# Performance work log

Measured on AMD Instinct MI355X. Metric: run time of the kernel, lower is better.

## Reference

```python
import jax, jax.numpy as jnp
import numpy as np

N_NODES = 100000
N_EDGES = 3200000
N_FEAT = 128
N_GRAPHS = 512


def setup_inputs() -> dict:
    key = jax.random.key(0)
    ks = jax.random.split(key, 12)
    x = jax.random.normal(ks[0], (N_NODES, N_FEAT), dtype=jnp.float32)
    edge_index = jax.random.randint(ks[1], (2, N_EDGES), 0, N_NODES, dtype=jnp.int64)
    batch = jnp.sort(jax.random.randint(ks[2], (N_NODES,), 0, N_GRAPHS, dtype=jnp.int64))
    s = 0.1
    return {
        "x": x,
        "edge_index": edge_index,
        "batch": batch,
        "W1": jax.random.normal(ks[3], (N_FEAT, 64), dtype=jnp.float32) * s,
        "b1": jnp.zeros((64,), dtype=jnp.float32),
        "W2": jax.random.normal(ks[4], (64, 64), dtype=jnp.float32) * s,
        "b2": jnp.zeros((64,), dtype=jnp.float32),
        "Wl1": jax.random.normal(ks[5], (64, 32), dtype=jnp.float32) * s,
        "bl1": jnp.zeros((32,), dtype=jnp.float32),
        "Wl2": jax.random.normal(ks[6], (32, 2), dtype=jnp.float32) * s,
        "bl2": jnp.zeros((2,), dtype=jnp.float32),
    }


def gcn_conv(x, src, dst, W, b, n_nodes):
    # PyG GCNConv: linear transform first, then symmetric-normalized
    # aggregation over A + I (self loops), bias added after aggregation.
    h = x @ W  # [N, out]
    loop = jnp.arange(n_nodes, dtype=src.dtype)
    s = jnp.concatenate([src, loop])
    d = jnp.concatenate([dst, loop])
    deg = jax.ops.segment_sum(jnp.ones(d.shape, dtype=h.dtype), d, num_segments=n_nodes)
    dinv = jax.lax.rsqrt(jnp.where(deg > 0, deg, 1.0))
    norm = dinv[s] * dinv[d]  # [E+N]
    msg = h[s] * norm[:, None]  # gather + scale
    out = jax.ops.segment_sum(msg, d, num_segments=n_nodes)  # scatter-add
    return out + b


def reference(x, edge_index, batch, W1, b1, W2, b2, Wl1, bl1, Wl2, bl2):
    src, dst = edge_index[0], edge_index[1]
    h = jax.nn.relu(gcn_conv(x, src, dst, W1, b1, N_NODES))
    # dropout is identity in eval mode
    h = gcn_conv(h, src, dst, W2, b2, N_NODES)
    # global mean pool over graphs
    counts = jax.ops.segment_sum(jnp.ones((N_NODES,), dtype=h.dtype), batch, num_segments=N_GRAPHS)
    pooled = jax.ops.segment_sum(h, batch, num_segments=N_GRAPHS)
    pooled = pooled / jnp.maximum(counts, 1.0)[:, None]  # [G, 64]
    z = pooled @ Wl1 + bl1
    z = z @ Wl2 + bl2  # [G, 2]
    return jax.nn.softmax(z, axis=0)  # faithful to Softmax(dim=0)
```

## Files before the change

kernel.cpp:

```cpp
#include <hip/hip_runtime.h>
#include <hip/hip_fp16.h>
#include <math.h>

#define N_NODES 100000
#define N_EDGES 3200000
#define N_GRAPHS 512

#define BSHIFT 8
#define BSPAN 256
#define NB 391
#define SLACK 9216
#define SBLK 4096
#define SBLOCKS ((N_EDGES + SBLK - 1) / SBLK)

typedef float floatx2 __attribute__((ext_vector_type(2)));

__global__ __launch_bounds__(512) void init_kernel(int* __restrict__ cursor) {
    int tid = threadIdx.x;
    if (tid < NB) cursor[tid] = tid * SLACK;
}

__global__ __launch_bounds__(256) void scatter3_kernel(const int* __restrict__ src,
                                                       const int* __restrict__ dst,
                                                       int* __restrict__ cursor,
                                                       unsigned int* __restrict__ pairs, int E) {
    __shared__ int hcnt[NB];
    __shared__ int hbase[NB];
    int tid = threadIdx.x;
    for (int b = tid; b < NB; b += 256) hcnt[b] = 0;
    __syncthreads();
    int base = blockIdx.x * SBLK;
    int end = min(E, base + SBLK);
    int e = base + tid * 4;
    for (; e + 3 < end; e += 1024) {
        int4 d4 = *reinterpret_cast<const int4*>(&dst[e]);
        atomicAdd(&hcnt[d4.x >> BSHIFT], 1);
        atomicAdd(&hcnt[d4.y >> BSHIFT], 1);
        atomicAdd(&hcnt[d4.z >> BSHIFT], 1);
        atomicAdd(&hcnt[d4.w >> BSHIFT], 1);
    }
    for (; e < end; ++e) atomicAdd(&hcnt[dst[e] >> BSHIFT], 1);
    __syncthreads();
    for (int b = tid; b < NB; b += 256) {
        int c = hcnt[b];
        if (c) hbase[b] = atomicAdd(&cursor[b], c);
        hcnt[b] = 0;
    }
    __syncthreads();
    e = base + tid * 4;
    for (; e + 3 < end; e += 1024) {
        int4 d4 = *reinterpret_cast<const int4*>(&dst[e]);
        int4 s4 = *reinterpret_cast<const int4*>(&src[e]);
        int b0 = d4.x >> BSHIFT, b1 = d4.y >> BSHIFT, b2 = d4.z >> BSHIFT, b3 = d4.w >> BSHIFT;
        int r0 = atomicAdd(&hcnt[b0], 1);
        int r1 = atomicAdd(&hcnt[b1], 1);
        int r2 = atomicAdd(&hcnt[b2], 1);
        int r3 = atomicAdd(&hcnt[b3], 1);
        pairs[hbase[b0] + r0] = ((unsigned int)s4.x << BSHIFT) | (unsigned int)(d4.x & (BSPAN - 1));
        pairs[hbase[b1] + r1] = ((unsigned int)s4.y << BSHIFT) | (unsigned int)(d4.y & (BSPAN - 1));
        pairs[hbase[b2] + r2] = ((unsigned int)s4.z << BSHIFT) | (unsigned int)(d4.z & (BSPAN - 1));
        pairs[hbase[b3] + r3] = ((unsigned int)s4.w << BSHIFT) | (unsigned int)(d4.w & (BSPAN - 1));
    }
    for (; e < end; ++e) {
        int d = dst[e];
        int b = d >> BSHIFT;
        int rk = atomicAdd(&hcnt[b], 1);
        pairs[hbase[b] + rk] = ((unsigned int)src[e] << BSHIFT) | (unsigned int)(d & (BSPAN - 1));
    }
}

__global__ __launch_bounds__(256) void bucket_kernel(const unsigned int* __restrict__ pairs,
                                                     const int* __restrict__ cursor,
                                                     int* __restrict__ col,
                                                     int2* __restrict__ bele,
                                                     float* __restrict__ dinv, int N) {
    __shared__ int ncnt[BSPAN];
    __shared__ int nb4[BSPAN];
    __shared__ int a[BSPAN];
    int b = blockIdx.x, tid = threadIdx.x;
    int base = b * SLACK;
    int cntb = cursor[b] - base;
    int n0 = b << BSHIFT;
    int nn = min(BSPAN, N - n0);
    ncnt[tid] = 0;
    __syncthreads();
    for (int i = tid; i < cntb; i += 256)
        atomicAdd(&ncnt[pairs[base + i] & (BSPAN - 1)], 1);
    __syncthreads();
    int v = ncnt[tid];
    int pad = (v + 3) & ~3;
    a[tid] = pad;
    __syncthreads();
    for (int st = 1; st < 256; st <<= 1) {
        int t = (tid >= st) ? a[tid - st] : 0;
        __syncthreads();
        a[tid] += t;
        __syncthreads();
    }
    int excl = a[tid] - pad;
    nb4[tid] = excl;
    if (tid < nn) {
        int beg = base + excl;
        bele[n0 + tid] = make_int2(beg, beg + v);
        dinv[n0 + tid] = rsqrtf((float)(v + 1));
    }
    ncnt[tid] = 0;
    __syncthreads();
    for (int i = tid; i < cntb; i += 256) {
        unsigned int p = pairs[base + i];
        int dl = p & (BSPAN - 1);
        int pos = base + nb4[dl] + atomicAdd(&ncnt[dl], 1);
        col[pos] = (int)(p >> BSHIFT) << 3;
    }
}

__global__ __launch_bounds__(128) void wz_kernel(const float* __restrict__ W2,
                                                 const float* __restrict__ b2,
                                                 const float* __restrict__ Wl1,
                                                 const float* __restrict__ bl1,
                                                 const float* __restrict__ Wl2,
                                                 const float* __restrict__ bl2,
                                                 float* __restrict__ Wz,
                                                 float* __restrict__ zc) {
    __shared__ float Weff[64 * 2];
    int tid = threadIdx.x;
    {
        int c = tid >> 1, j = tid & 1;
        float s = 0.f;
        for (int k = 0; k < 32; ++k) s += Wl1[c * 32 + k] * Wl2[k * 2 + j];
        Weff[c * 2 + j] = s;
    }
    __syncthreads();
    {
        int i = tid >> 1, j = tid & 1;
        float s = 0.f;
        for (int c = 0; c < 64; ++c) s += W2[i * 64 + c] * Weff[c * 2 + j];
        Wz[i * 2 + j] = s;
    }
    if (tid < 2) {
        float s = bl2[tid];
        for (int k = 0; k < 32; ++k) s += bl1[k] * Wl2[k * 2 + tid];
        for (int c = 0; c < 64; ++c) s += b2[c] * Weff[c * 2 + tid];
        zc[tid] = s;
    }
}

template <int K>
__global__ __launch_bounds__(256) void lin_kernel(const float* __restrict__ X,
                                                  const float* __restrict__ W,
                                                  const float* __restrict__ rs,
                                                  unsigned char* __restrict__ U) {
    __shared__ float Ws[K * 64];
    __shared__ float Xs[32 * K];
    int tid = threadIdx.x;
    for (int i = tid * 4; i < K * 64; i += 256 * 4)
        *reinterpret_cast<float4*>(&Ws[i]) = *reinterpret_cast<const float4*>(&W[i]);
    int row0 = blockIdx.x * 32;
    const float* Xbase = X + (size_t)row0 * K;
    for (int i = tid * 4; i < 32 * K; i += 256 * 4)
        *reinterpret_cast<float4*>(&Xs[i]) = *reinterpret_cast<const float4*>(&Xbase[i]);
    __syncthreads();

    int wid = tid >> 6, lane = tid & 63;
    int rbase = wid * 8;
    float acc[8];
#pragma unroll
    for (int r = 0; r < 8; ++r) acc[r] = 0.f;

    for (int k4 = 0; k4 < K / 4; ++k4) {
        float w0 = Ws[(k4 * 4 + 0) * 64 + lane];
        float w1 = Ws[(k4 * 4 + 1) * 64 + lane];
        float w2 = Ws[(k4 * 4 + 2) * 64 + lane];
        float w3 = Ws[(k4 * 4 + 3) * 64 + lane];
#pragma unroll
        for (int r = 0; r < 8; ++r) {
            float4 xv = *reinterpret_cast<const float4*>(&Xs[(rbase + r) * K + k4 * 4]);
            acc[r] += xv.x * w0 + xv.y * w1 + xv.z * w2 + xv.w * w3;
        }
    }
#pragma unroll
    for (int r = 0; r < 8; ++r) {
        int row = row0 + rbase + r;
        float v = acc[r] * rs[row];
        int pk = __builtin_amdgcn_cvt_pk_fp8_f32(v, v, 0, false);
        U[(size_t)row * 64 + lane] = (unsigned char)(pk & 0xff);
    }
}

#define ACC8(a)                                                                  \
    {                                                                            \
        acc2[0] += __builtin_amdgcn_cvt_pk_f32_fp8((int)(a).x, false);           \
        acc2[1] += __builtin_amdgcn_cvt_pk_f32_fp8((int)(a).x, true);            \
        acc2[2] += __builtin_amdgcn_cvt_pk_f32_fp8((int)(a).y, false);           \
        acc2[3] += __builtin_amdgcn_cvt_pk_f32_fp8((int)(a).y, true);            \
    }

__global__ __launch_bounds__(256) void agg1_kernel(const unsigned char* __restrict__ u,
                                                   const int2* __restrict__ bele,
                                                   const int* __restrict__ col,
                                                   const float* __restrict__ dinv,
                                                   const float* __restrict__ bias,
                                                   const float* __restrict__ Wz,
                                                   float2* __restrict__ qz, int n) {
    __shared__ float Wz0s[64];
    __shared__ float Wz1s[64];
    int tid = threadIdx.x;
    if (tid < 64) Wz0s[tid] = Wz[tid * 2];
    else if (tid < 128) Wz1s[tid - 64] = Wz[(tid - 64) * 2 + 1];
    __syncthreads();

    int wid = tid >> 6, lane = tid & 63;
    int node = blockIdx.x * 4 + wid;
    if (node >= n) return;
    int r = lane >> 3, c = lane & 7;
    unsigned int c8 = (unsigned int)c * 8;

    int2 be = bele[node];
    int beg = be.x, end = be.y;
    floatx2 acc2[4];
#pragma unroll
    for (int j = 0; j < 4; ++j) acc2[j] = (floatx2)(0.f);

    int e = beg + r * 4;
    while (e + 3 < end) {
        int4 c4 = *reinterpret_cast<const int4*>(&col[e]);
        uint2 a0 = *reinterpret_cast<const uint2*>(u + (((unsigned int)c4.x << 3) + c8));
        uint2 a1 = *reinterpret_cast<const uint2*>(u + (((unsigned int)c4.y << 3) + c8));
        uint2 a2 = *reinterpret_cast<const uint2*>(u + (((unsigned int)c4.z << 3) + c8));
        uint2 a3 = *reinterpret_cast<const uint2*>(u + (((unsigned int)c4.w << 3) + c8));
        ACC8(a0); ACC8(a1); ACC8(a2); ACC8(a3);
        e += 32;
    }
#pragma unroll
    for (int k = 0; k < 4; ++k) {
        int ee = e + k;
        if (ee < end) {
            uint2 a0 = *reinterpret_cast<const uint2*>(u + (((unsigned int)col[ee] << 3) + c8));
            ACC8(a0);
        }
    }
#pragma unroll
    for (int m = 8; m <= 32; m <<= 1) {
#pragma unroll
        for (int j = 0; j < 4; ++j) {
            acc2[j].x += __shfl_xor(acc2[j].x, m);
            acc2[j].y += __shfl_xor(acc2[j].y, m);
        }
    }
    if (r == 0) {
        unsigned int vs = ((unsigned int)node << 6) + c8;
        uint2 sfr = *reinterpret_cast<const uint2*>(u + vs);
        ACC8(sfr);
        float di = dinv[node];
        float4 b0 = *reinterpret_cast<const float4*>(&bias[c * 8]);
        float4 b1 = *reinterpret_cast<const float4*>(&bias[c * 8 + 4]);
        float o[8];
#pragma unroll
        for (int j = 0; j < 4; ++j) {
            o[2 * j]     = di * acc2[j].x;
            o[2 * j + 1] = di * acc2[j].y;
        }
        o[0] += b0.x; o[1] += b0.y; o[2] += b0.z; o[3] += b0.w;
        o[4] += b1.x; o[5] += b1.y; o[6] += b1.z; o[7] += b1.w;
#pragma unroll
        for (int j = 0; j < 8; ++j) o[j] = fmaxf(o[j], 0.f);
        float p0 = 0.f, p1 = 0.f;
#pragma unroll
        for (int j = 0; j < 8; ++j) {
            p0 += o[j] * Wz0s[c * 8 + j];
            p1 += o[j] * Wz1s[c * 8 + j];
        }
#pragma unroll
        for (int m = 1; m <= 4; m <<= 1) {
            p0 += __shfl_xor(p0, m);
            p1 += __shfl_xor(p1, m);
        }
        if (lane == 0) qz[node] = make_float2(p0 * di, p1 * di);
    }
}

__global__ __launch_bounds__(256) void agg2q_kernel(const float2* __restrict__ qz,
                                                    const int2* __restrict__ bele,
                                                    const int* __restrict__ col,
                                                    const float* __restrict__ dinv,
                                                    float* __restrict__ pooled2,
                                                    const int* __restrict__ batch, int n) {
    __shared__ float2 sh[16];
    __shared__ int sg[16];
    int tid = threadIdx.x;
    int wid = tid >> 6, lane = tid & 63;
    int sub = lane >> 4, slot = lane & 15;
    int li = wid * 4 + sub;
    int node = blockIdx.x * 16 + li;
    bool valid = node < n;

    float ax = 0.f, ay = 0.f;
    if (valid) {
        int2 be = bele[node];
        const char* qb = (const char*)qz;
        int e = be.x + slot;
        while (e + 16 < be.y) {
            float2 v0 = *reinterpret_cast<const float2*>(qb + (unsigned int)col[e]);
            float2 v1 = *reinterpret_cast<const float2*>(qb + (unsigned int)col[e + 16]);
            ax += v0.x + v1.x; ay += v0.y + v1.y;
            e += 32;
        }
        if (e < be.y) {
            float2 v0 = *reinterpret_cast<const float2*>(qb + (unsigned int)col[e]);
            ax += v0.x; ay += v0.y;
        }
    }
#pragma unroll
    for (int m = 1; m <= 8; m <<= 1) {
        ax += __shfl_xor(ax, m);
        ay += __shfl_xor(ay, m);
    }
    if (slot == 0) {
        if (valid) {
            float2 self = qz[node];
            float di = dinv[node];
            sh[li] = make_float2(di * (ax + self.x), di * (ay + self.y));
            sg[li] = batch[node];
        } else {
            sh[li] = make_float2(0.f, 0.f);
            sg[li] = -1;
        }
    }
    __syncthreads();
    if (tid < 2) {
        float s = 0.f;
        int gp = -1;
        for (int w = 0; w < 16; ++w) {
            int g = sg[w];
            if (g < 0) continue;
            if (g != gp) {
                if (gp >= 0) atomicAdd(&pooled2[gp * 2 + tid], s);
                s = 0.f;
                gp = g;
            }
            s += (tid == 0) ? sh[w].x : sh[w].y;
        }
        if (gp >= 0) atomicAdd(&pooled2[gp * 2 + tid], s);
    }
}

__global__ __launch_bounds__(512) void head_kernel(const float* __restrict__ pooled2,
                                                   const int* __restrict__ batch,
                                                   const float* __restrict__ zc,
                                                   float* __restrict__ out, int N) {
    __shared__ float red[512];
    int tid = threadIdx.x;
    int g = tid;
    auto lb = [&](int key) {
        int l = 0, r = N;
        while (l < r) { int m = (l + r) >> 1; if (batch[m] < key) l = m + 1; else r = m; }
        return l;
    };
    int cnt = lb(g + 1) - lb(g);
    float cn = fmaxf((float)cnt, 1.f);
    float z0 = pooled2[g * 2 + 0] / cn + zc[0];
    float z1 = pooled2[g * 2 + 1] / cn + zc[1];

    red[tid] = z0; __syncthreads();
    for (int s = 256; s > 0; s >>= 1) { if (tid < s) red[tid] = fmaxf(red[tid], red[tid + s]); __syncthreads(); }
    float m0 = red[0]; __syncthreads();
    float e0 = expf(z0 - m0);
    red[tid] = e0; __syncthreads();
    for (int s = 256; s > 0; s >>= 1) { if (tid < s) red[tid] += red[tid + s]; __syncthreads(); }
    float s0 = red[0]; __syncthreads();
    out[g * 2 + 0] = e0 / s0;

    red[tid] = z1; __syncthreads();
    for (int s = 256; s > 0; s >>= 1) { if (tid < s) red[tid] = fmaxf(red[tid], red[tid + s]); __syncthreads(); }
    float m1 = red[0]; __syncthreads();
    float e1 = expf(z1 - m1);
    red[tid] = e1; __syncthreads();
    for (int s = 256; s > 0; s >>= 1) { if (tid < s) red[tid] += red[tid + s]; __syncthreads(); }
    float s1 = red[0]; __syncthreads();
    out[g * 2 + 1] = e1 / s1;
}

extern "C" void kernel_launch(void* const* d_in, const int* in_sizes, int n_in,
                              void* d_out, int out_size, void* d_ws, size_t ws_size,
                              hipStream_t stream) {
    const float* x   = (const float*)d_in[0];
    const int*   ei  = (const int*)d_in[1];
    const int*   bat = (const int*)d_in[2];
    const float* W1  = (const float*)d_in[3];
    const float* b1  = (const float*)d_in[4];
    const float* W2  = (const float*)d_in[5];
    const float* b2  = (const float*)d_in[6];
    const float* Wl1 = (const float*)d_in[7];
    const float* bl1 = (const float*)d_in[8];
    const float* Wl2 = (const float*)d_in[9];
    const float* bl2 = (const float*)d_in[10];
    float* out = (float*)d_out;

    const int N = N_NODES, E = N_EDGES;
    const int* src = ei;
    const int* dst = ei + E;

    size_t o = 0;
    auto alloc = [&](size_t bytes) {
        void* p = (char*)d_ws + o;
        o += (bytes + 255) / 256 * 256;
        return p;
    };
    int*           cursor  = (int*)alloc((size_t)NB * 4);
    unsigned int*  pairs   = (unsigned int*)alloc((size_t)NB * SLACK * 4 + 4096);
    int*           col     = (int*)alloc((size_t)NB * SLACK * 4 + 4096);
    int2*          bele    = (int2*)alloc((size_t)N * 8);
    float*         dinv    = (float*)alloc((size_t)N * 4);
    unsigned char* T       = (unsigned char*)alloc((size_t)N * 64);
    float2*        qz      = (float2*)alloc((size_t)N * 8);
    float*         Wz      = (float*)alloc(128 * 4);
    float*         zc      = (float*)alloc(2 * 4);
    float*         pooled2 = (float*)alloc((size_t)N_GRAPHS * 2 * 4);

    hipMemsetAsync(pooled2, 0, (size_t)N_GRAPHS * 2 * 4, stream);

    init_kernel<<<1, 512, 0, stream>>>(cursor);
    scatter3_kernel<<<SBLOCKS, 256, 0, stream>>>(src, dst, cursor, pairs, E);
    bucket_kernel<<<NB, 256, 0, stream>>>(pairs, cursor, col, bele, dinv, N);

    wz_kernel<<<1, 128, 0, stream>>>(W2, b2, Wl1, bl1, Wl2, bl2, Wz, zc);

    lin_kernel<128><<<N / 32, 256, 0, stream>>>(x, W1, dinv, T);
    agg1_kernel<<<(N + 3) / 4, 256, 0, stream>>>(T, bele, col, dinv, b1, Wz, qz, N);

    agg2q_kernel<<<(N + 15) / 16, 256, 0, stream>>>(qz, bele, col, dinv, pooled2, bat, N);

    head_kernel<<<1, 512, 0, stream>>>(pooled2, bat, zc, out, N);
}
```

Measured before the change: 225.8 us.

## Shrink CSR buckets, single-pass register-held scatter, and strided edge loop in aggregation

Halves the destination bucket span to 128 nodes (782 buckets, smaller slack), so the bucket kernel gets more blocks and less per-block work. The scatter kernel now loads dst and src once into registers and keeps the local atomic ranks, which removes the second read pass and the second round of shared atomics. Per-node column padding to multiples of 4 is dropped, and agg1 now reads edges strided by 8 across lanes instead of int4 chunks. The risks are more register pressure in scatter, a slack overflow if a bucket exceeds 4800 edges, and scalar col loads in place of vector ones.

Result: faster. 218.9 us (-3.1%).

```diff
diff --git a/kernel.cpp b/kernel.cpp
--- a/kernel.cpp
+++ b/kernel.cpp
@@ -6,18 +6,18 @@
 #define N_EDGES 3200000
 #define N_GRAPHS 512
 
-#define BSHIFT 8
-#define BSPAN 256
-#define NB 391
-#define SLACK 9216
+#define BSHIFT 7
+#define BSPAN 128
+#define NB 782
+#define SLACK 4800
 #define SBLK 4096
 #define SBLOCKS ((N_EDGES + SBLK - 1) / SBLK)
 
 typedef float floatx2 __attribute__((ext_vector_type(2)));
 
 __global__ __launch_bounds__(512) void init_kernel(int* __restrict__ cursor) {
-    int tid = threadIdx.x;
-    if (tid < NB) cursor[tid] = tid * SLACK;
+    int i = blockIdx.x * 512 + threadIdx.x;
+    if (i < NB) cursor[i] = i * SLACK;
 }
 
 __global__ __launch_bounds__(256) void scatter3_kernel(const int* __restrict__ src,
@@ -31,41 +31,45 @@
     __syncthreads();
     int base = blockIdx.x * SBLK;
     int end = min(E, base + SBLK);
-    int e = base + tid * 4;
-    for (; e + 3 < end; e += 1024) {
-        int4 d4 = *reinterpret_cast<const int4*>(&dst[e]);
-        atomicAdd(&hcnt[d4.x >> BSHIFT], 1);
-        atomicAdd(&hcnt[d4.y >> BSHIFT], 1);
-        atomicAdd(&hcnt[d4.z >> BSHIFT], 1);
-        atomicAdd(&hcnt[d4.w >> BSHIFT], 1);
-    }
-    for (; e < end; ++e) atomicAdd(&hcnt[dst[e] >> BSHIFT], 1);
+    int4 dv[4], sv[4];
+    int rk[16];
+    bool ok[4];
+#pragma unroll
+    for (int k = 0; k < 4; ++k) {
+        int e = base + tid * 4 + k * 1024;
+        ok[k] = (e < end);
+        if (ok[k]) {
+            dv[k] = *reinterpret_cast<const int4*>(&dst[e]);
+            sv[k] = *reinterpret_cast<const int4*>(&src[e]);
+        }
+    }
+#pragma unroll
+    for (int k = 0; k < 4; ++k) {
+        if (ok[k]) {
+            rk[4 * k + 0] = atomicAdd(&hcnt[dv[k].x >> BSHIFT], 1);
+            rk[4 * k + 1] = atomicAdd(&hcnt[dv[k].y >> BSHIFT], 1);
+            rk[4 * k + 2] = atomicAdd(&hcnt[dv[k].z >> BSHIFT], 1);
+            rk[4 * k + 3] = atomicAdd(&hcnt[dv[k].w >> BSHIFT], 1);
+        }
+    }
     __syncthreads();
     for (int b = tid; b < NB; b += 256) {
         int c = hcnt[b];
         if (c) hbase[b] = atomicAdd(&cursor[b], c);
-        hcnt[b] = 0;
-    }
-    __syncthreads();
-    e = base + tid * 4;
-    for (; e + 3 < end; e += 1024) {
-        int4 d4 = *reinterpret_cast<const int4*>(&dst[e]);
-        int4 s4 = *reinterpret_cast<const int4*>(&src[e]);
-        int b0 = d4.x >> BSHIFT, b1 = d4.y >> BSHIFT, b2 = d4.z >> BSHIFT, b3 = d4.w >> BSHIFT;
-        int r0 = atomicAdd(&hcnt[b0], 1);
-        int r1 = atomicAdd(&hcnt[b1], 1);
-        int r2 = atomicAdd(&hcnt[b2], 1);
-        int r3 = atomicAdd(&hcnt[b3], 1);
-        pairs[hbase[b0] + r0] = ((unsigned int)s4.x << BSHIFT) | (unsigned int)(d4.x & (BSPAN - 1));
-        pairs[hbase[b1] + r1] = ((unsigned int)s4.y << BSHIFT) | (unsigned int)(d4.y & (BSPAN - 1));
-        pairs[hbase[b2] + r2] = ((unsigned int)s4.z << BSHIFT) | (unsigned int)(d4.z & (BSPAN - 1));
-        pairs[hbase[b3] + r3] = ((unsigned int)s4.w << BSHIFT) | (unsigned int)(d4.w & (BSPAN - 1));
-    }
-    for (; e < end; ++e) {
-        int d = dst[e];
-        int b = d >> BSHIFT;
-        int rk = atomicAdd(&hcnt[b], 1);
-        pairs[hbase[b] + rk] = ((unsigned int)src[e] << BSHIFT) | (unsigned int)(d & (BSPAN - 1));
+    }
+    __syncthreads();
+#pragma unroll
+    for (int k = 0; k < 4; ++k) {
+        if (ok[k]) {
+            pairs[hbase[dv[k].x >> BSHIFT] + rk[4 * k + 0]] =
+                ((unsigned int)sv[k].x << BSHIFT) | (unsigned int)(dv[k].x & (BSPAN - 1));
+            pairs[hbase[dv[k].y >> BSHIFT] + rk[4 * k + 1]] =
+                ((unsigned int)sv[k].y << BSHIFT) | (unsigned int)(dv[k].y & (BSPAN - 1));
+            pairs[hbase[dv[k].z >> BSHIFT] + rk[4 * k + 2]] =
+                ((unsigned int)sv[k].z << BSHIFT) | (unsigned int)(dv[k].z & (BSPAN - 1));
+            pairs[hbase[dv[k].w >> BSHIFT] + rk[4 * k + 3]] =
+                ((unsigned int)sv[k].w << BSHIFT) | (unsigned int)(dv[k].w & (BSPAN - 1));
+        }
     }
 }
 
@@ -75,41 +79,45 @@
                                                      int2* __restrict__ bele,
                                                      float* __restrict__ dinv, int N) {
     __shared__ int ncnt[BSPAN];
-    __shared__ int nb4[BSPAN];
+    __shared__ int nbase[BSPAN];
     __shared__ int a[BSPAN];
     int b = blockIdx.x, tid = threadIdx.x;
     int base = b * SLACK;
     int cntb = cursor[b] - base;
     int n0 = b << BSHIFT;
     int nn = min(BSPAN, N - n0);
-    ncnt[tid] = 0;
+    if (tid < BSPAN) ncnt[tid] = 0;
     __syncthreads();
     for (int i = tid; i < cntb; i += 256)
         atomicAdd(&ncnt[pairs[base + i] & (BSPAN - 1)], 1);
     __syncthreads();
-    int v = ncnt[tid];
-    int pad = (v + 3) & ~3;
-    a[tid] = pad;
-    __syncthreads();
-    for (int st = 1; st < 256; st <<= 1) {
-        int t = (tid >= st) ? a[tid - st] : 0;
+    if (tid < BSPAN) {
+        int v = ncnt[tid];
+        a[tid] = v;
+    }
+    __syncthreads();
+    for (int st = 1; st < BSPAN; st <<= 1) {
+        int t = (tid < BSPAN && tid >= st) ? a[tid - st] : 0;
         __syncthreads();
-        a[tid] += t;
+        if (tid < BSPAN) a[tid] += t;
         __syncthreads();
     }
-    int excl = a[tid] - pad;
-    nb4[tid] = excl;
-    if (tid < nn) {
-        int beg = base + excl;
-        bele[n0 + tid] = make_int2(beg, beg + v);
-        dinv[n0 + tid] = rsqrtf((float)(v + 1));
-    }
-    ncnt[tid] = 0;
+    if (tid < BSPAN) {
+        int v = ncnt[tid];
+        int excl = a[tid] - v;
+        nbase[tid] = excl;
+        if (tid < nn) {
+            int beg = base + excl;
+            bele[n0 + tid] = make_int2(beg, beg + v);
+            dinv[n0 + tid] = rsqrtf((float)(v + 1));
+        }
+        ncnt[tid] = 0;
+    }
     __syncthreads();
     for (int i = tid; i < cntb; i += 256) {
         unsigned int p = pairs[base + i];
         int dl = p & (BSPAN - 1);
-        int pos = base + nb4[dl] + atomicAdd(&ncnt[dl], 1);
+        int pos = base + nbase[dl] + atomicAdd(&ncnt[dl], 1);
         col[pos] = (int)(p >> BSHIFT) << 3;
     }
 }
@@ -221,23 +229,31 @@
 #pragma unroll
     for (int j = 0; j < 4; ++j) acc2[j] = (floatx2)(0.f);
 
-    int e = beg + r * 4;
-    while (e + 3 < end) {
-        int4 c4 = *reinterpret_cast<const int4*>(&col[e]);
-        uint2 a0 = *reinterpret_cast<const uint2*>(u + (((unsigned int)c4.x << 3) + c8));
-        uint2 a1 = *reinterpret_cast<const uint2*>(u + (((unsigned int)c4.y << 3) + c8));
-        uint2 a2 = *reinterpret_cast<const uint2*>(u + (((unsigned int)c4.z << 3) + c8));
-        uint2 a3 = *reinterpret_cast<const uint2*>(u + (((unsigned int)c4.w << 3) + c8));
+    int e = beg + r;
+    while (e + 24 < end) {
+        unsigned int v0 = ((unsigned int)col[e]      << 3) + c8;
+        unsigned int v1 = ((unsigned int)col[e + 8]  << 3) + c8;
+        unsigned int v2 = ((unsigned int)col[e + 16] << 3) + c8;
+        unsigned int v3 = ((unsigned int)col[e + 24] << 3) + c8;
+        uint2 a0 = *reinterpret_cast<const uint2*>(u + v0);
+        uint2 a1 = *reinterpret_cast<const uint2*>(u + v1);
+        uint2 a2 = *reinterpret_cast<const uint2*>(u + v2);
+        uint2 a3 = *reinterpret_cast<const uint2*>(u + v3);
         ACC8(a0); ACC8(a1); ACC8(a2); ACC8(a3);
         e += 32;
     }
-#pragma unroll
-    for (int k = 0; k < 4; ++k) {
-        int ee = e + k;
-        if (ee < end) {
-            uint2 a0 = *reinterpret_cast<const uint2*>(u + (((unsigned int)col[ee] << 3) + c8));
-            ACC8(a0);
-        }
+    while (e + 8 < end) {
+        unsigned int v0 = ((unsigned int)col[e]     << 3) + c8;
+        unsigned int v1 = ((unsigned int)col[e + 8] << 3) + c8;
+        uint2 a0 = *reinterpret_cast<const uint2*>(u + v0);
+        uint2 a1 = *reinterpret_cast<const uint2*>(u + v1);
+        ACC8(a0); ACC8(a1);
+        e += 16;
+    }
+    if (e < end) {
+        unsigned int v0 = ((unsigned int)col[e] << 3) + c8;
+        uint2 a0 = *reinterpret_cast<const uint2*>(u + v0);
+        ACC8(a0);
     }
 #pragma unroll
     for (int m = 8; m <= 32; m <<= 1) {
@@ -419,7 +435,7 @@
 
     hipMemsetAsync(pooled2, 0, (size_t)N_GRAPHS * 2 * 4, stream);
 
-    init_kernel<<<1, 512, 0, stream>>>(cursor);
+    init_kernel<<<(NB + 511) / 512, 512, 0, stream>>>(cursor);
     scatter3_kernel<<<SBLOCKS, 256, 0, stream>>>(src, dst, cursor, pairs, E);
     bucket_kernel<<<NB, 256, 0, stream>>>(pairs, cursor, col, bele, dinv, N);
 
```
